# Optimization experiments

Hardware: AMD Instinct MI355X
Metric: run time of the kernel (lower is better)

## Reference

```python
import jax, jax.numpy as jnp
import numpy as np

EPS = 1e-5

def _bn(h, gamma, beta):
    # BatchNorm1d in training mode: per-channel stats over the batch dim (L=1)
    m = jnp.mean(h, axis=0)
    v = jnp.var(h, axis=0)  # biased variance, as torch uses for normalization
    return gamma * (h - m) * jax.lax.rsqrt(v + EPS) + beta

def setup_inputs() -> dict:
    key = jax.random.key(0)
    ks = jax.random.split(key, 8)
    vocab, emb = 8192, 512
    inter = (vocab + emb) // 2  # 4352
    N = 8192
    x_t = jax.random.randint(ks[0], (N,), 0, vocab, dtype=jnp.int64)
    W1 = jax.random.normal(ks[1], (inter, vocab), dtype=jnp.float32) * 0.02
    b1 = jax.random.normal(ks[2], (inter,), dtype=jnp.float32) * 0.02
    g1 = jnp.ones((inter,), dtype=jnp.float32)
    beta1 = jnp.zeros((inter,), dtype=jnp.float32)
    W2 = jax.random.normal(ks[3], (emb, inter), dtype=jnp.float32) * 0.02
    b2 = jax.random.normal(ks[4], (emb,), dtype=jnp.float32) * 0.02
    g2 = jnp.ones((emb,), dtype=jnp.float32)
    beta2 = jnp.zeros((emb,), dtype=jnp.float32)
    return {"x_t": x_t, "W1": W1, "b1": b1, "g1": g1, "beta1": beta1,
            "W2": W2, "b2": b2, "g2": g2, "beta2": beta2}

def reference(x_t, W1, b1, g1, beta1, W2, b2, g2, beta2):
    # one_hot(x_t) @ Conv1d(k=1) weight == gather of W1 columns (same math, no dense one-hot)
    h1 = W1.T[x_t] + b1                      # [N, inter]
    h1 = jax.nn.gelu(_bn(h1, g1, beta1), approximate=False)
    h2 = h1 @ W2.T + b2                      # [N, emb]
    out = jax.nn.gelu(_bn(h2, g2, beta2), approximate=False)
    return out
```

## Files before the change

kernel.cpp:

```cpp
#include <hip/hip_runtime.h>
#include <hip/hip_bf16.h>
#include <math.h>

typedef __attribute__((ext_vector_type(8))) short short8;
typedef __attribute__((ext_vector_type(4))) float f32x4;

#define VOCAB 8192
#define NSAMP 8192
#define INTER 4352
#define EMB   512

#define OFF_CNT    0
#define OFF_A1     32768
#define OFF_M1     50176
#define OFF_S1     67584
#define OFF_S2     84992
#define OFF_A2     102400
#define OFF_M2     104448
#define OFF_PS1B   106496
#define OFF_PS2B   1155072
#define OFF_W2B    2203648
#define OFF_HACT   6660096
#define OFF_HPART  77963264
#define PART_BYTES 16777216ULL

__device__ __forceinline__ float gelu_exact(float x) {
    return 0.5f * x * (1.0f + erff(x * 0.70710678118654752f));
}
__device__ __forceinline__ unsigned short f2bf(float x) {
    __hip_bfloat16 b = __float2bfloat16(x);
    return *reinterpret_cast<unsigned short*>(&b);
}
__device__ __forceinline__ void async16(const unsigned short* g, unsigned short* l) {
    __builtin_amdgcn_global_load_lds(
        (const __attribute__((address_space(1))) void*)g,
        (__attribute__((address_space(3))) void*)l, 16, 0, 0);
}

__global__ void k_zero_cnt(int* cnt) {
    cnt[blockIdx.x * 256 + threadIdx.x] = 0;
}
__global__ void k_hist(const int* __restrict__ xt, int* __restrict__ cnt) {
    int n = blockIdx.x * 256 + threadIdx.x;
    atomicAdd(&cnt[xt[n]], 1);
}

__global__ __launch_bounds__(256) void k_stats1(const float* __restrict__ W1,
                                                const int* __restrict__ cnt,
                                                float* __restrict__ s1o,
                                                float* __restrict__ s2o) {
    const int t = threadIdx.x, lane = t & 63, w = t >> 6;
    const int row = blockIdx.x * 4 + w;
    const float* wr = W1 + (size_t)row * VOCAB;
    float s1 = 0.f, s2 = 0.f;
    #pragma unroll 8
    for (int it = 0; it < 32; ++it) {
        int v = it * 256 + lane * 4;
        float4 x = *(const float4*)(wr + v);
        int4 c = *(const int4*)(cnt + v);
        float cx = (float)c.x, cy = (float)c.y, cz = (float)c.z, cw = (float)c.w;
        s1 += cx * x.x + cy * x.y + cz * x.z + cw * x.w;
        s2 += cx * x.x * x.x + cy * x.y * x.y + cz * x.z * x.z + cw * x.w * x.w;
    }
    #pragma unroll
    for (int d = 1; d < 64; d <<= 1) {
        s1 += __shfl_xor(s1, d);
        s2 += __shfl_xor(s2, d);
    }
    if (lane == 0) { s1o[row] = s1; s2o[row] = s2; }
}

__global__ void k_stats1f(const float* __restrict__ s1, const float* __restrict__ s2,
                          const float* __restrict__ g1, float* __restrict__ a1,
                          float* __restrict__ m1) {
    int i = blockIdx.x * 256 + threadIdx.x;
    float m = s1[i] * (1.f / NSAMP);
    float var = s2[i] * (1.f / NSAMP) - m * m;
    a1[i] = g1[i] * rsqrtf(var + 1e-5f);
    m1[i] = m;
}

__global__ __launch_bounds__(256) void k_build(const float* __restrict__ W1,
                                               const float* __restrict__ a1,
                                               const float* __restrict__ m1,
                                               const float* __restrict__ beta1,
                                               unsigned short* __restrict__ Hact) {
    const int i0 = blockIdx.x * 64;
    const int v0 = blockIdx.y * 256;
    const int t = threadIdx.x;
    const int c0 = (t & 15) * 4;
    const int vg = (t >> 4) * 4;
    float4 av = *(const float4*)(a1 + i0 + c0);
    float4 mv = *(const float4*)(m1 + i0 + c0);
    float4 bv = *(const float4*)(beta1 + i0 + c0);
    const float* ap = (const float*)&av;
    const float* mp = (const float*)&mv;
    const float* bp = (const float*)&bv;
    #pragma unroll
    for (int vi = 0; vi < 4; ++vi) {
        int vb = v0 + vi * 64 + vg;
        float wf[4][4];
        #pragma unroll
        for (int j = 0; j < 4; ++j)
            *(float4*)&wf[j][0] = *(const float4*)(W1 + (size_t)(i0 + c0 + j) * VOCAB + vb);
        #pragma unroll
        for (int k = 0; k < 4; ++k) {
            ushort4 o;
            o.x = f2bf(gelu_exact(ap[0] * (wf[0][k] - mp[0]) + bp[0]));
            o.y = f2bf(gelu_exact(ap[1] * (wf[1][k] - mp[1]) + bp[1]));
            o.z = f2bf(gelu_exact(ap[2] * (wf[2][k] - mp[2]) + bp[2]));
            o.w = f2bf(gelu_exact(ap[3] * (wf[3][k] - mp[3]) + bp[3]));
            *(ushort4*)&Hact[(size_t)(vb + k) * INTER + i0 + c0] = o;
        }
    }
}

__global__ void k_w2bf(const float* __restrict__ W2, unsigned short* __restrict__ W2b) {
    int idx = (blockIdx.x * 256 + threadIdx.x) * 4;
    float4 w = *(const float4*)(W2 + idx);
    ushort4 u;
    u.x = f2bf(w.x); u.y = f2bf(w.y); u.z = f2bf(w.z); u.w = f2bf(w.w);
    *(ushort4*)(W2b + idx) = u;
}

__global__ __launch_bounds__(256) void k_gemm(const unsigned short* __restrict__ A,
                                              const unsigned short* __restrict__ B,
                                              float* __restrict__ Cp, int kPer) {
    __shared__ __align__(16) unsigned short sA[128 * 64];
    __shared__ __align__(16) unsigned short sB[128 * 64];
    const int m0 = blockIdx.x * 128;
    const int n0 = blockIdx.y * 128;
    const int kbeg = blockIdx.z * kPer;
    const int kend = kbeg + kPer;
    float* C = Cp + (size_t)blockIdx.z * NSAMP * EMB;
    const int t = threadIdx.x;
    const int lane = t & 63;
    const int wave = t >> 6;
    const int wr = wave >> 1, wc = wave & 1;
    const int mq = lane & 15, kq = lane >> 4;
    const int srow = lane >> 3;
    const int scol = (lane & 7) * 8;
    f32x4 acc[4][4];
    #pragma unroll
    for (int r = 0; r < 4; ++r)
        #pragma unroll
        for (int c = 0; c < 4; ++c) acc[r][c] = (f32x4){0.f, 0.f, 0.f, 0.f};
    for (int k0 = kbeg; k0 < kend; k0 += 64) {
        #pragma unroll
        for (int p = 0; p < 4; ++p) {
            int r0 = (p * 4 + wave) * 8;
            async16(A + (size_t)(m0 + r0 + srow) * INTER + k0 + scol, &sA[r0 * 64]);
            async16(B + (size_t)(n0 + r0 + srow) * INTER + k0 + scol, &sB[r0 * 64]);
        }
        __syncthreads();
        #pragma unroll
        for (int kk = 0; kk < 64; kk += 32) {
            short8 af[4], bf[4];
            #pragma unroll
            for (int r = 0; r < 4; ++r)
                af[r] = *(const short8*)&sA[(wr * 64 + r * 16 + mq) * 64 + kk + kq * 8];
            #pragma unroll
            for (int c = 0; c < 4; ++c)
                bf[c] = *(const short8*)&sB[(wc * 64 + c * 16 + mq) * 64 + kk + kq * 8];
            #pragma unroll
            for (int r = 0; r < 4; ++r)
                #pragma unroll
                for (int c = 0; c < 4; ++c)
                    acc[r][c] = __builtin_amdgcn_mfma_f32_16x16x32_bf16(af[r], bf[c], acc[r][c], 0, 0, 0);
        }
        __syncthreads();
    }
    #pragma unroll
    for (int r = 0; r < 4; ++r) {
        #pragma unroll
        for (int c = 0; c < 4; ++c) {
            int col = n0 + wc * 64 + c * 16 + mq;
            int rowb = m0 + wr * 64 + r * 16 + kq * 4;
            #pragma unroll
            for (int j = 0; j < 4; ++j)
                C[(size_t)(rowb + j) * EMB + col] = acc[r][c][j];
        }
    }
}

__global__ __launch_bounds__(256) void k_reduce(const float* hpart,
                                                const int* __restrict__ cnt,
                                                float* h2,
                                                float* __restrict__ ps1,
                                                float* __restrict__ ps2, int S) {
    __shared__ float4 b1[128], b2[128];
    const int v0 = blockIdx.x * 16;
    const int t = threadIdx.x;
    const int half = t >> 7;
    const int c4 = (t & 127) * 4;
    float4 acc1 = {0.f, 0.f, 0.f, 0.f}, acc2 = {0.f, 0.f, 0.f, 0.f};
    #pragma unroll
    for (int rp = 0; rp < 8; ++rp) {
        int v = v0 + rp * 2 + half;
        size_t off = (size_t)v * EMB + c4;
        float4 h = *(const float4*)(hpart + off);
        for (int s = 1; s < S; ++s) {
            float4 hs = *(const float4*)(hpart + (size_t)s * NSAMP * EMB + off);
            h.x += hs.x; h.y += hs.y; h.z += hs.z; h.w += hs.w;
        }
        *(float4*)(h2 + off) = h;
        float w = (float)cnt[v];
        acc1.x += w * h.x; acc1.y += w * h.y; acc1.z += w * h.z; acc1.w += w * h.w;
        acc2.x += w * h.x * h.x; acc2.y += w * h.y * h.y;
        acc2.z += w * h.z * h.z; acc2.w += w * h.w * h.w;
    }
    if (half == 1) { b1[t & 127] = acc1; b2[t & 127] = acc2; }
    __syncthreads();
    if (half == 0) {
        float4 o1 = b1[t & 127], o2 = b2[t & 127];
        o1.x += acc1.x; o1.y += acc1.y; o1.z += acc1.z; o1.w += acc1.w;
        o2.x += acc2.x; o2.y += acc2.y; o2.z += acc2.z; o2.w += acc2.w;
        ps1[(size_t)(c4 + 0) * 512 + blockIdx.x] = o1.x;
        ps1[(size_t)(c4 + 1) * 512 + blockIdx.x] = o1.y;
        ps1[(size_t)(c4 + 2) * 512 + blockIdx.x] = o1.z;
        ps1[(size_t)(c4 + 3) * 512 + blockIdx.x] = o1.w;
        ps2[(size_t)(c4 + 0) * 512 + blockIdx.x] = o2.x;
        ps2[(size_t)(c4 + 1) * 512 + blockIdx.x] = o2.y;
        ps2[(size_t)(c4 + 2) * 512 + blockIdx.x] = o2.z;
        ps2[(size_t)(c4 + 3) * 512 + blockIdx.x] = o2.w;
    }
}

__global__ __launch_bounds__(256) void k_stats2f(const float* __restrict__ ps1,
                                                 const float* __restrict__ ps2,
                                                 const float* __restrict__ g2,
                                                 float* __restrict__ a2,
                                                 float* __restrict__ m2) {
    const int lane = threadIdx.x & 63;
    const int e = blockIdx.x * 4 + (threadIdx.x >> 6);
    float s1 = 0.f, s2 = 0.f;
    #pragma unroll
    for (int k = 0; k < 8; ++k) {
        s1 += ps1[(size_t)e * 512 + k * 64 + lane];
        s2 += ps2[(size_t)e * 512 + k * 64 + lane];
    }
    #pragma unroll
    for (int d = 1; d < 64; d <<= 1) {
        s1 += __shfl_xor(s1, d);
        s2 += __shfl_xor(s2, d);
    }
    if (lane == 0) {
        float m = s1 * (1.f / NSAMP);
        float var = s2 * (1.f / NSAMP) - m * m;
        a2[e] = g2[e] * rsqrtf(var + 1e-5f);
        m2[e] = m;
    }
}

__global__ __launch_bounds__(256) void k_final(const float* __restrict__ h2,
                                               const int* __restrict__ xt,
                                               const float* __restrict__ a2,
                                               const float* __restrict__ m2,
                                               const float* __restrict__ beta2,
                                               float* __restrict__ out) {
    const int t = threadIdx.x;
    const int n = blockIdx.x * 2 + (t >> 7);
    const int e = (t & 127) * 4;
    const int v = xt[n];
    float4 h = *(const float4*)(h2 + (size_t)v * EMB + e);
    float4 a = *(const float4*)(a2 + e);
    float4 m = *(const float4*)(m2 + e);
    float4 b = *(const float4*)(beta2 + e);
    float4 o;
    o.x = gelu_exact(a.x * (h.x - m.x) + b.x);
    o.y = gelu_exact(a.y * (h.y - m.y) + b.y);
    o.z = gelu_exact(a.z * (h.z - m.z) + b.z);
    o.w = gelu_exact(a.w * (h.w - m.w) + b.w);
    *(float4*)(out + (size_t)n * EMB + e) = o;
}

extern "C" void kernel_launch(void* const* d_in, const int* in_sizes, int n_in,
                              void* d_out, int out_size, void* d_ws, size_t ws_size,
                              hipStream_t stream) {
    const int* xt      = (const int*)d_in[0];
    const float* W1    = (const float*)d_in[1];
    const float* g1    = (const float*)d_in[3];
    const float* beta1 = (const float*)d_in[4];
    const float* W2    = (const float*)d_in[5];
    const float* g2    = (const float*)d_in[7];
    const float* beta2 = (const float*)d_in[8];
    float* out = (float*)d_out;

    char* ws = (char*)d_ws;
    int*   cnt  = (int*)  (ws + OFF_CNT);
    float* a1   = (float*)(ws + OFF_A1);
    float* m1   = (float*)(ws + OFF_M1);
    float* s1   = (float*)(ws + OFF_S1);
    float* s2   = (float*)(ws + OFF_S2);
    float* a2   = (float*)(ws + OFF_A2);
    float* m2   = (float*)(ws + OFF_M2);
    float* ps1b = (float*)(ws + OFF_PS1B);
    float* ps2b = (float*)(ws + OFF_PS2B);
    unsigned short* W2b  = (unsigned short*)(ws + OFF_W2B);
    unsigned short* Hact = (unsigned short*)(ws + OFF_HACT);
    float* hpart = (float*)(ws + OFF_HPART);
    float* h2 = hpart;

    int S = 1;
    if (ws_size >= OFF_HPART + 4 * PART_BYTES) S = 4;
    else if (ws_size >= OFF_HPART + 2 * PART_BYTES) S = 2;

    k_zero_cnt<<<32, 256, 0, stream>>>(cnt);
    k_hist<<<32, 256, 0, stream>>>(xt, cnt);
    k_stats1<<<1088, 256, 0, stream>>>(W1, cnt, s1, s2);
    k_stats1f<<<17, 256, 0, stream>>>(s1, s2, g1, a1, m1);
    k_build<<<dim3(68, 32), 256, 0, stream>>>(W1, a1, m1, beta1, Hact);
    k_w2bf<<<2176, 256, 0, stream>>>(W2, W2b);
    k_gemm<<<dim3(64, 4, S), 256, 0, stream>>>(Hact, W2b, hpart, INTER / S);
    k_reduce<<<512, 256, 0, stream>>>(hpart, cnt, h2, ps1b, ps2b, S);
    k_stats2f<<<128, 256, 0, stream>>>(ps1b, ps2b, g2, a2, m2);
    k_final<<<4096, 256, 0, stream>>>(h2, xt, a2, m2, beta2, out);
}
```

Baseline: 369.5 us.

## Compact used vocab rows so GEMM and reduce skip unused tokens

Adds a single-block prefix-scan kernel that assigns a dense rank to each vocab id that appears in x_t. The activation build writes only used rows at their compacted rank, the GEMM exits early for row tiles past the used count, and the reduce and final kernels index through the rank map. With 8192 random samples over 8192 vocab entries only about 63% of ids appear, so roughly a third of the GEMM tiles and reduce work are dropped. It also folds the stats1 finalize into stats1 to remove one launch, at the cost of a serial 1024-thread scan kernel.

New measurement: 392.7 us. +6.3%, slower.

```diff
diff --git a/kernel.cpp b/kernel.cpp
--- a/kernel.cpp
+++ b/kernel.cpp
@@ -11,18 +11,21 @@
 #define EMB   512
 
 #define OFF_CNT    0
-#define OFF_A1     32768
-#define OFF_M1     50176
-#define OFF_S1     67584
-#define OFF_S2     84992
-#define OFF_A2     102400
-#define OFF_M2     104448
-#define OFF_PS1B   106496
-#define OFF_PS2B   1155072
-#define OFF_W2B    2203648
-#define OFF_HACT   6660096
-#define OFF_HPART  77963264
+#define OFF_RANK   32768
+#define OFF_CNTC   65536
+#define OFF_NUSED  98304
+#define OFF_A1     98368
+#define OFF_M1     115776
+#define OFF_A2     133184
+#define OFF_M2     135232
+#define OFF_PS1B   137280
+#define OFF_PS2B   1185856
+#define OFF_W2B    2234432
+#define OFF_HACT   6690880
+#define OFF_HPART  77994048
 #define PART_BYTES 16777216ULL
+
+#define RSENT 0xFFFFFFFFu
 
 __device__ __forceinline__ float gelu_exact(float x) {
     return 0.5f * x * (1.0f + erff(x * 0.70710678118654752f));
@@ -45,10 +48,51 @@
     atomicAdd(&cnt[xt[n]], 1);
 }
 
+__global__ __launch_bounds__(1024) void k_scan(const int* __restrict__ cnt,
+                                               unsigned int* __restrict__ rank,
+                                               int* __restrict__ cntc,
+                                               int* __restrict__ nUsed) {
+    __shared__ int tsum[1024];
+    const int t = threadIdx.x;
+    const int base = t * 8;
+    int c[8], f[8];
+    int4 a = *(const int4*)(cnt + base);
+    int4 b = *(const int4*)(cnt + base + 4);
+    c[0]=a.x; c[1]=a.y; c[2]=a.z; c[3]=a.w; c[4]=b.x; c[5]=b.y; c[6]=b.z; c[7]=b.w;
+    int s = 0;
+    #pragma unroll
+    for (int j = 0; j < 8; ++j) { f[j] = s; s += (c[j] > 0); }
+    tsum[t] = s;
+    __syncthreads();
+    #pragma unroll
+    for (int d = 1; d < 1024; d <<= 1) {
+        int v = (t >= d) ? tsum[t - d] : 0;
+        __syncthreads();
+        tsum[t] += v;
+        __syncthreads();
+    }
+    const int excl = (t == 0) ? 0 : tsum[t - 1];
+    *(int4*)(cntc + base) = (int4){0,0,0,0};
+    *(int4*)(cntc + base + 4) = (int4){0,0,0,0};
+    __syncthreads();
+    #pragma unroll
+    for (int j = 0; j < 8; ++j) {
+        if (c[j] > 0) {
+            unsigned int r = (unsigned int)(excl + f[j]);
+            rank[base + j] = r;
+            cntc[r] = c[j];
+        } else {
+            rank[base + j] = RSENT;
+        }
+    }
+    if (t == 1023) nUsed[0] = tsum[1023];
+}
+
 __global__ __launch_bounds__(256) void k_stats1(const float* __restrict__ W1,
                                                 const int* __restrict__ cnt,
-                                                float* __restrict__ s1o,
-                                                float* __restrict__ s2o) {
+                                                const float* __restrict__ g1,
+                                                float* __restrict__ a1,
+                                                float* __restrict__ m1) {
     const int t = threadIdx.x, lane = t & 63, w = t >> 6;
     const int row = blockIdx.x * 4 + w;
     const float* wr = W1 + (size_t)row * VOCAB;
@@ -67,23 +111,19 @@
         s1 += __shfl_xor(s1, d);
         s2 += __shfl_xor(s2, d);
     }
-    if (lane == 0) { s1o[row] = s1; s2o[row] = s2; }
-}
-
-__global__ void k_stats1f(const float* __restrict__ s1, const float* __restrict__ s2,
-                          const float* __restrict__ g1, float* __restrict__ a1,
-                          float* __restrict__ m1) {
-    int i = blockIdx.x * 256 + threadIdx.x;
-    float m = s1[i] * (1.f / NSAMP);
-    float var = s2[i] * (1.f / NSAMP) - m * m;
-    a1[i] = g1[i] * rsqrtf(var + 1e-5f);
-    m1[i] = m;
+    if (lane == 0) {
+        float m = s1 * (1.f / NSAMP);
+        float var = s2 * (1.f / NSAMP) - m * m;
+        a1[row] = g1[row] * rsqrtf(var + 1e-5f);
+        m1[row] = m;
+    }
 }
 
 __global__ __launch_bounds__(256) void k_build(const float* __restrict__ W1,
                                                const float* __restrict__ a1,
                                                const float* __restrict__ m1,
                                                const float* __restrict__ beta1,
+                                               const unsigned int* __restrict__ rank,
                                                unsigned short* __restrict__ Hact) {
     const int i0 = blockIdx.x * 64;
     const int v0 = blockIdx.y * 256;
@@ -105,12 +145,15 @@
             *(float4*)&wf[j][0] = *(const float4*)(W1 + (size_t)(i0 + c0 + j) * VOCAB + vb);
         #pragma unroll
         for (int k = 0; k < 4; ++k) {
-            ushort4 o;
-            o.x = f2bf(gelu_exact(ap[0] * (wf[0][k] - mp[0]) + bp[0]));
-            o.y = f2bf(gelu_exact(ap[1] * (wf[1][k] - mp[1]) + bp[1]));
-            o.z = f2bf(gelu_exact(ap[2] * (wf[2][k] - mp[2]) + bp[2]));
-            o.w = f2bf(gelu_exact(ap[3] * (wf[3][k] - mp[3]) + bp[3]));
-            *(ushort4*)&Hact[(size_t)(vb + k) * INTER + i0 + c0] = o;
+            unsigned int rk = rank[vb + k];
+            if (rk != RSENT) {
+                ushort4 o;
+                o.x = f2bf(gelu_exact(ap[0] * (wf[0][k] - mp[0]) + bp[0]));
+                o.y = f2bf(gelu_exact(ap[1] * (wf[1][k] - mp[1]) + bp[1]));
+                o.z = f2bf(gelu_exact(ap[2] * (wf[2][k] - mp[2]) + bp[2]));
+                o.w = f2bf(gelu_exact(ap[3] * (wf[3][k] - mp[3]) + bp[3]));
+                *(ushort4*)&Hact[(size_t)rk * INTER + i0 + c0] = o;
+            }
         }
     }
 }
@@ -125,10 +168,12 @@
 
 __global__ __launch_bounds__(256) void k_gemm(const unsigned short* __restrict__ A,
                                               const unsigned short* __restrict__ B,
-                                              float* __restrict__ Cp, int kPer) {
+                                              float* __restrict__ Cp, int kPer,
+                                              const int* __restrict__ nUsed) {
+    const int m0 = blockIdx.x * 128;
+    if (m0 >= nUsed[0]) return;
     __shared__ __align__(16) unsigned short sA[128 * 64];
     __shared__ __align__(16) unsigned short sB[128 * 64];
-    const int m0 = blockIdx.x * 128;
     const int n0 = blockIdx.y * 128;
     const int kbeg = blockIdx.z * kPer;
     const int kend = kbeg + kPer;
@@ -184,7 +229,7 @@
 }
 
 __global__ __launch_bounds__(256) void k_reduce(const float* hpart,
-                                                const int* __restrict__ cnt,
+                                                const int* __restrict__ cntc,
                                                 float* h2,
                                                 float* __restrict__ ps1,
                                                 float* __restrict__ ps2, int S) {
@@ -196,18 +241,21 @@
     float4 acc1 = {0.f, 0.f, 0.f, 0.f}, acc2 = {0.f, 0.f, 0.f, 0.f};
     #pragma unroll
     for (int rp = 0; rp < 8; ++rp) {
-        int v = v0 + rp * 2 + half;
-        size_t off = (size_t)v * EMB + c4;
-        float4 h = *(const float4*)(hpart + off);
-        for (int s = 1; s < S; ++s) {
-            float4 hs = *(const float4*)(hpart + (size_t)s * NSAMP * EMB + off);
-            h.x += hs.x; h.y += hs.y; h.z += hs.z; h.w += hs.w;
-        }
-        *(float4*)(h2 + off) = h;
-        float w = (float)cnt[v];
-        acc1.x += w * h.x; acc1.y += w * h.y; acc1.z += w * h.z; acc1.w += w * h.w;
-        acc2.x += w * h.x * h.x; acc2.y += w * h.y * h.y;
-        acc2.z += w * h.z * h.z; acc2.w += w * h.w * h.w;
+        int r = v0 + rp * 2 + half;
+        int cw_i = cntc[r];
+        if (cw_i > 0) {
+            size_t off = (size_t)r * EMB + c4;
+            float4 h = *(const float4*)(hpart + off);
+            for (int s = 1; s < S; ++s) {
+                float4 hs = *(const float4*)(hpart + (size_t)s * NSAMP * EMB + off);
+                h.x += hs.x; h.y += hs.y; h.z += hs.z; h.w += hs.w;
+            }
+            *(float4*)(h2 + off) = h;
+            float w = (float)cw_i;
+            acc1.x += w * h.x; acc1.y += w * h.y; acc1.z += w * h.z; acc1.w += w * h.w;
+            acc2.x += w * h.x * h.x; acc2.y += w * h.y * h.y;
+            acc2.z += w * h.z * h.z; acc2.w += w * h.w * h.w;
+        }
     }
     if (half == 1) { b1[t & 127] = acc1; b2[t & 127] = acc2; }
     __syncthreads();
@@ -254,6 +302,7 @@
 
 __global__ __launch_bounds__(256) void k_final(const float* __restrict__ h2,
                                                const int* __restrict__ xt,
+                                               const unsigned int* __restrict__ rank,
                                                const float* __restrict__ a2,
                                                const float* __restrict__ m2,
                                                const float* __restrict__ beta2,
@@ -261,8 +310,8 @@
     const int t = threadIdx.x;
     const int n = blockIdx.x * 2 + (t >> 7);
     const int e = (t & 127) * 4;
-    const int v = xt[n];
-    float4 h = *(const float4*)(h2 + (size_t)v * EMB + e);
+    const unsigned int rk = rank[xt[n]];
+    float4 h = *(const float4*)(h2 + (size_t)rk * EMB + e);
     float4 a = *(const float4*)(a2 + e);
     float4 m = *(const float4*)(m2 + e);
     float4 b = *(const float4*)(beta2 + e);
@@ -288,10 +337,11 @@
 
     char* ws = (char*)d_ws;
     int*   cnt  = (int*)  (ws + OFF_CNT);
+    unsigned int* rank = (unsigned int*)(ws + OFF_RANK);
+    int*   cntc = (int*)  (ws + OFF_CNTC);
+    int*   nUsed= (int*)  (ws + OFF_NUSED);
     float* a1   = (float*)(ws + OFF_A1);
     float* m1   = (float*)(ws + OFF_M1);
-    float* s1   = (float*)(ws + OFF_S1);
-    float* s2   = (float*)(ws + OFF_S2);
     float* a2   = (float*)(ws + OFF_A2);
     float* m2   = (float*)(ws + OFF_M2);
     float* ps1b = (float*)(ws + OFF_PS1B);
@@ -307,12 +357,12 @@
 
     k_zero_cnt<<<32, 256, 0, stream>>>(cnt);
     k_hist<<<32, 256, 0, stream>>>(xt, cnt);
-    k_stats1<<<1088, 256, 0, stream>>>(W1, cnt, s1, s2);
-    k_stats1f<<<17, 256, 0, stream>>>(s1, s2, g1, a1, m1);
-    k_build<<<dim3(68, 32), 256, 0, stream>>>(W1, a1, m1, beta1, Hact);
+    k_scan<<<1, 1024, 0, stream>>>(cnt, rank, cntc, nUsed);
+    k_stats1<<<1088, 256, 0, stream>>>(W1, cnt, g1, a1, m1);
+    k_build<<<dim3(68, 32), 256, 0, stream>>>(W1, a1, m1, beta1, rank, Hact);
     k_w2bf<<<2176, 256, 0, stream>>>(W2, W2b);
-    k_gemm<<<dim3(64, 4, S), 256, 0, stream>>>(Hact, W2b, hpart, INTER / S);
-    k_reduce<<<512, 256, 0, stream>>>(hpart, cnt, h2, ps1b, ps2b, S);
+    k_gemm<<<dim3(64, 4, S), 256, 0, stream>>>(Hact, W2b, hpart, INTER / S, nUsed);
+    k_reduce<<<512, 256, 0, stream>>>(hpart, cntc, h2, ps1b, ps2b, S);
     k_stats2f<<<128, 256, 0, stream>>>(ps1b, ps2b, g2, a2, m2);
-    k_final<<<4096, 256, 0, stream>>>(h2, xt, a2, m2, beta2, out);
-}
+    k_final<<<4096, 256, 0, stream>>>(h2, xt, rank, a2, m2, beta2, out);
+}
```
